# Kernel tuning notes

Hardware: AMD Instinct MI355X
Metric: run time of the kernel (lower is better)

The kernel has to match this reference:

```python
import jax, jax.numpy as jnp
import numpy as np

SCALE = 64.0
MARGIN = 0.5
COS_M = float(np.cos(MARGIN))
SIN_M = float(np.sin(MARGIN))
TH = float(np.cos(np.pi - MARGIN))
MM = float(np.sin(np.pi - MARGIN) * MARGIN)
B, D, C = 1024, 512, 50000


def setup_inputs() -> dict:
    key = jax.random.key(0)
    k1, k2, k3 = jax.random.split(key, 3)
    embeddings = jax.random.normal(k1, (B, D), dtype=jnp.float32)
    labels = jax.random.randint(k2, (B,), 0, C, dtype=jnp.int32)
    # xavier_uniform over (num_classes, embedding_dim)
    limit = float(np.sqrt(6.0 / (C + D)))
    weight = jax.random.uniform(k3, (C, D), dtype=jnp.float32, minval=-limit, maxval=limit)
    return {"embeddings": embeddings, "labels": labels, "weight": weight}


def _l2norm(x, axis=-1, eps=1e-12):
    # matches F.normalize(p=2): x / max(||x||, eps)
    n = jnp.sqrt(jnp.sum(x * x, axis=axis, keepdims=True))
    return x / jnp.maximum(n, eps)


def reference(embeddings, labels, weight):
    e = _l2norm(embeddings, axis=1)          # [B, D]
    w = _l2norm(weight, axis=1)              # [C, D]
    cosine = jnp.einsum('bd,cd->bc', e, w)   # [B, C]
    sine = jnp.sqrt(1.0 - jnp.clip(cosine * cosine, 0.0, 1.0))
    phi = cosine * COS_M - sine * SIN_M
    phi = jnp.where(cosine > TH, phi, cosine - MM)
    one_hot = jax.nn.one_hot(labels, cosine.shape[1], dtype=cosine.dtype)
    logits = SCALE * (one_hot * phi + (1.0 - one_hot) * cosine)
    # cross_entropy with integer labels, mean reduction
    logp = jax.nn.log_softmax(logits, axis=1)
    nll = -jnp.take_along_axis(logp, labels[:, None].astype(jnp.int32), axis=1)[:, 0]
    return jnp.mean(nll)
```

## Files before the change

### kernel.cpp

```cpp
#include <hip/hip_runtime.h>
#include <hip/hip_bf16.h>
#include <cstdint>

#define BB 1024
#define DD 512
#define CC 50000
#define CCP 50048
#define NTN 782
#define NBLK 512
#define SCALE_F 64.0f
#define LOG2E_F 1.44269504088896340736f
#define SCALE_L2E_F (SCALE_F * LOG2E_F)
#define COS_M_F 0.87758256189037276f
#define SIN_M_F 0.47942553860420301f
#define TH_F   (-0.87758256189037276f)
#define MM_F   0.23971276930210156f

typedef __attribute__((ext_vector_type(4))) int i32x4;
typedef __attribute__((ext_vector_type(8))) char char8;

#define OFF_RS   ((size_t)0)
#define OFF_ES   (OFF_RS + 4096)
#define OFF_WS   (OFF_ES + 4096)
#define OFF_EI8  (OFF_WS + 204800)
#define OFF_WI8  (OFF_EI8 + (size_t)BB*DD)

__global__ void quant_kernel(const float* __restrict__ emb, const float* __restrict__ wgt,
                             char* __restrict__ ei8, float* __restrict__ es,
                             char* __restrict__ wi8, float* __restrict__ wsc,
                             float* __restrict__ rowsum, float* __restrict__ out) {
    const int blk = blockIdx.x;
    if (blk == 12756) {
        const int t = threadIdx.x;
        #pragma unroll
        for (int i = 0; i < 4; ++i) rowsum[i * 256 + t] = 0.f;
        if (t == 0) out[0] = 0.f;
        int4* pz = reinterpret_cast<int4*>(wi8 + (size_t)CC * DD + t * 96);
        #pragma unroll
        for (int i = 0; i < 6; ++i) pz[i] = (int4){0, 0, 0, 0};
        if (t < CCP - CC) wsc[CC + t] = 0.f;
        return;
    }
    const int r4 = threadIdx.x >> 6;
    const int l  = threadIdx.x & 63;
    const bool isw = blk < 12500;
    const int row = isw ? (blk * 4 + r4) : ((blk - 12500) * 4 + r4);
    const float* src = (isw ? wgt : emb) + (size_t)row * DD;
    const float4* r = reinterpret_cast<const float4*>(src);
    float4 v0 = r[l * 2 + 0];
    float4 v1 = r[l * 2 + 1];
    float ss = v0.x*v0.x + v0.y*v0.y + v0.z*v0.z + v0.w*v0.w
             + v1.x*v1.x + v1.y*v1.y + v1.z*v1.z + v1.w*v1.w;
    float mx = fmaxf(fmaxf(fmaxf(fabsf(v0.x), fabsf(v0.y)), fmaxf(fabsf(v0.z), fabsf(v0.w))),
                     fmaxf(fmaxf(fabsf(v1.x), fabsf(v1.y)), fmaxf(fabsf(v1.z), fabsf(v1.w))));
    #pragma unroll
    for (int m = 1; m < 64; m <<= 1) {
        ss += __shfl_xor(ss, m);
        mx = fmaxf(mx, __shfl_xor(mx, m));
    }
    float nrm = fmaxf(sqrtf(ss), 1e-12f);
    float ma  = fmaxf(mx, 1e-20f);
    float qs  = 127.0f / ma;
    if (l == 0) (isw ? wsc : es)[row] = ma / (127.0f * nrm);
    char8 q;
    q[0]=(char)__float2int_rn(v0.x*qs); q[1]=(char)__float2int_rn(v0.y*qs);
    q[2]=(char)__float2int_rn(v0.z*qs); q[3]=(char)__float2int_rn(v0.w*qs);
    q[4]=(char)__float2int_rn(v1.x*qs); q[5]=(char)__float2int_rn(v1.y*qs);
    q[6]=(char)__float2int_rn(v1.z*qs); q[7]=(char)__float2int_rn(v1.w*qs);
    *reinterpret_cast<char8*>((isw ? wi8 : ei8) + (size_t)row * DD + l * 8) = q;
}

__global__ __launch_bounds__(512, 4) void arc_gemm_i8_kernel(
        const char* __restrict__ ei8,
        const char* __restrict__ wi8,
        const float* __restrict__ es,
        const float* __restrict__ wsc,
        float* __restrict__ rowsum)
{
    __shared__ __align__(16) char lds[2][32768];

    const int t   = threadIdx.x;
    const int wid = t >> 6;
    const int wm  = wid >> 1;
    const int wn  = wid & 1;
    const int l   = t & 63;
    const int r16 = l & 15;
    const int kg  = l >> 4;

    const int bid  = blockIdx.x;
    const int bidp = (bid & 7) * 64 + (bid >> 3);
    const int mt = bidp & 7;
    const int s  = bidp >> 3;
    const int m0 = mt * 128;
    const int nt0 = (s < 14) ? s * 13 : 12 * s + 14;
    const int cnt = (s < 14) ? 13 : 12;

    i32x4 af[2][8];
    #pragma unroll
    for (int fm = 0; fm < 2; ++fm)
        #pragma unroll
        for (int kk = 0; kk < 8; ++kk)
            af[fm][kk] = *reinterpret_cast<const i32x4*>(
                ei8 + (size_t)(m0 + wm * 32 + fm * 16 + r16) * DD + kk * 64 + kg * 16);

    float se_r[2][4];
    #pragma unroll
    for (int fm = 0; fm < 2; ++fm)
        #pragma unroll
        for (int j = 0; j < 4; ++j)
            se_r[fm][j] = es[m0 + wm * 32 + fm * 16 + kg * 4 + j];

    float rs[2][4];
    #pragma unroll
    for (int fm = 0; fm < 2; ++fm)
        #pragma unroll
        for (int j = 0; j < 4; ++j) rs[fm][j] = 0.f;

    const char* sp4[4];
    #pragma unroll
    for (int i = 0; i < 4; ++i) {
        int flat = (i * 512 + t) * 16;
        int kk2  = flat >> 13;
        int row  = (flat >> 7) & 63;
        int col  = flat & 127;
        int scol = col ^ ((row & 7) << 4);
        sp4[i] = wi8 + (size_t)(nt0 * 64 + row) * DD + kk2 * 128 + scol;
    }
    auto stageB = [&](int buf) {
        #pragma unroll
        for (int i = 0; i < 4; ++i) {
            __builtin_amdgcn_global_load_lds(
                (const __attribute__((address_space(1))) void*)sp4[i],
                (__attribute__((address_space(3))) void*)(&lds[buf][(i * 512 + t) * 16]),
                16, 0, 0);
            sp4[i] += 64 * DD;
        }
    };
    const float* wp = wsc + nt0 * 64 + wn * 32 + r16;

    stageB(0);
    asm volatile("s_waitcnt vmcnt(0)" ::: "memory");
    __builtin_amdgcn_s_barrier();

    for (int i = 0; i < cnt; ++i) {
        const int buf = i & 1;
        if (i + 1 < cnt) stageB(buf ^ 1);

        float sw_0 = wp[0]  * SCALE_L2E_F;
        float sw_1 = wp[16] * SCALE_L2E_F;
        wp += 64;

        i32x4 acc[2][2];
        #pragma unroll
        for (int fm = 0; fm < 2; ++fm)
            #pragma unroll
            for (int fn = 0; fn < 2; ++fn) acc[fm][fn] = (i32x4){0, 0, 0, 0};
        #pragma unroll
        for (int kk = 0; kk < 8; ++kk) {
            i32x4 b[2];
            #pragma unroll
            for (int fn = 0; fn < 2; ++fn) {
                int row = wn * 32 + fn * 16 + r16;
                int off = (kk >> 1) * 8192 + row * 128
                        + (((kk & 1) * 64 + kg * 16) ^ ((row & 7) << 4));
                b[fn] = *reinterpret_cast<const i32x4*>(&lds[buf][off]);
            }
            #pragma unroll
            for (int fm = 0; fm < 2; ++fm)
                #pragma unroll
                for (int fn = 0; fn < 2; ++fn)
                    acc[fm][fn] = __builtin_amdgcn_mfma_i32_16x16x64_i8(af[fm][kk], b[fn], acc[fm][fn], 0, 0, 0);
        }

        asm volatile("s_waitcnt vmcnt(0)" ::: "memory");
        __builtin_amdgcn_s_barrier();

        #pragma unroll
        for (int fm = 0; fm < 2; ++fm)
            #pragma unroll
            for (int j = 0; j < 4; ++j) {
                float k0 = se_r[fm][j] * sw_0;
                float k1 = se_r[fm][j] * sw_1;
                rs[fm][j] += exp2f(fmaf((float)acc[fm][0][j], k0, -SCALE_L2E_F));
                rs[fm][j] += exp2f(fmaf((float)acc[fm][1][j], k1, -SCALE_L2E_F));
            }
    }

    #pragma unroll
    for (int fm = 0; fm < 2; ++fm) {
        #pragma unroll
        for (int j = 0; j < 4; ++j) {
            float v = rs[fm][j];
            #pragma unroll
            for (int mk = 1; mk < 16; mk <<= 1) v += __shfl_xor(v, mk);
            if (r16 == 0) {
                int grow = m0 + wm * 32 + fm * 16 + kg * 4 + j;
                atomicAdd(&rowsum[grow], v);
            }
        }
    }
}

__global__ void finish_kernel(const char* __restrict__ ei8, const char* __restrict__ wi8,
                              const float* __restrict__ es, const float* __restrict__ wsc,
                              const int* __restrict__ labels,
                              const float* __restrict__ rowsum, float* __restrict__ out) {
    const int b = blockIdx.x;
    const int l = threadIdx.x;
    const int lab = labels[b];
    char8 a = *reinterpret_cast<const char8*>(ei8 + (size_t)b * DD + l * 8);
    char8 w = *reinterpret_cast<const char8*>(wi8 + (size_t)lab * DD + l * 8);
    int d = 0;
    #pragma unroll
    for (int k = 0; k < 8; ++k) d += (int)a[k] * (int)w[k];
    #pragma unroll
    for (int m = 1; m < 64; m <<= 1) d += __shfl_xor(d, m);
    if (l == 0) {
        float swl = wsc[lab] * SCALE_L2E_F;
        float kf  = es[b] * swl;
        float sub = exp2f(fmaf((float)d, kf, -SCALE_L2E_F));
        float cosv = (float)d * es[b] * wsc[lab];
        float c2 = fminf(fmaxf(cosv * cosv, 0.f), 1.f);
        float phi = cosv * COS_M_F - sqrtf(1.f - c2) * SIN_M_F;
        phi = (cosv > TH_F) ? phi : (cosv - MM_F);
        float ml = SCALE_F * phi;
        float Sf = rowsum[b] + __expf(ml - SCALE_F) - sub;
        float nll = -(ml - SCALE_F - logf(Sf));
        atomicAdd(out, nll * (1.0f / BB));
    }
}

extern "C" void kernel_launch(void* const* d_in, const int* in_sizes, int n_in,
                              void* d_out, int out_size, void* d_ws, size_t ws_size,
                              hipStream_t stream) {
    const float* emb    = (const float*)d_in[0];
    const int*   labels = (const int*)d_in[1];
    const float* wgt    = (const float*)d_in[2];
    float* out = (float*)d_out;
    char* ws = (char*)d_ws;

    float* rowsum = (float*)(ws + OFF_RS);
    float* es     = (float*)(ws + OFF_ES);
    float* wsc    = (float*)(ws + OFF_WS);
    char*  ei8    = (char*)(ws + OFF_EI8);
    char*  wi8    = (char*)(ws + OFF_WI8);

    quant_kernel<<<12757, 256, 0, stream>>>(emb, wgt, ei8, es, wi8, wsc, rowsum, out);
    arc_gemm_i8_kernel<<<NBLK, 512, 0, stream>>>(ei8, wi8, es, wsc, rowsum);
    finish_kernel<<<BB, 64, 0, stream>>>(ei8, wi8, es, wsc, labels, rowsum, out);
}
```

Before: 81.74 us.

## Drop LDS staging; load B fragments directly from global with smaller blocks

The GEMM kernel no longer stages weight tiles through double-buffered LDS with global_load_lds and barriers. Each wave now reads its B fragments straight from global memory into registers. Blocks shrink to 256 threads covering 32-column tiles, and the grid doubles to 1024 blocks. This removes LDS traffic and block-wide synchronisation, but there is no longer any prefetch overlap, and every wave in a block re-reads the same weight rows from global or L2 instead of sharing them.

```diff
diff --git a/kernel.cpp b/kernel.cpp
--- a/kernel.cpp
+++ b/kernel.cpp
@@ -6,8 +6,8 @@
 #define DD 512
 #define CC 50000
 #define CCP 50048
-#define NTN 782
-#define NBLK 512
+#define NCT 1564
+#define NBLK 1024
 #define SCALE_F 64.0f
 #define LOG2E_F 1.44269504088896340736f
 #define SCALE_L2E_F (SCALE_F * LOG2E_F)
@@ -70,30 +70,26 @@
     *reinterpret_cast<char8*>((isw ? wi8 : ei8) + (size_t)row * DD + l * 8) = q;
 }
 
-__global__ __launch_bounds__(512, 4) void arc_gemm_i8_kernel(
+__global__ __launch_bounds__(256, 4) void arc_gemm_i8_kernel(
         const char* __restrict__ ei8,
         const char* __restrict__ wi8,
         const float* __restrict__ es,
         const float* __restrict__ wsc,
         float* __restrict__ rowsum)
 {
-    __shared__ __align__(16) char lds[2][32768];
-
     const int t   = threadIdx.x;
     const int wid = t >> 6;
-    const int wm  = wid >> 1;
-    const int wn  = wid & 1;
     const int l   = t & 63;
     const int r16 = l & 15;
     const int kg  = l >> 4;
 
     const int bid  = blockIdx.x;
-    const int bidp = (bid & 7) * 64 + (bid >> 3);
+    const int bidp = (bid & 7) * 128 + (bid >> 3);
     const int mt = bidp & 7;
     const int s  = bidp >> 3;
-    const int m0 = mt * 128;
-    const int nt0 = (s < 14) ? s * 13 : 12 * s + 14;
-    const int cnt = (s < 14) ? 13 : 12;
+    const int rowb = mt * 128 + wid * 32;
+    const int nt0 = (s < 28) ? s * 13 : 12 * s + 28;
+    const int cnt = (s < 28) ? 13 : 12;
 
     i32x4 af[2][8];
     #pragma unroll
@@ -101,14 +97,14 @@
         #pragma unroll
         for (int kk = 0; kk < 8; ++kk)
             af[fm][kk] = *reinterpret_cast<const i32x4*>(
-                ei8 + (size_t)(m0 + wm * 32 + fm * 16 + r16) * DD + kk * 64 + kg * 16);
+                ei8 + (size_t)(rowb + fm * 16 + r16) * DD + kk * 64 + kg * 16);
 
     float se_r[2][4];
     #pragma unroll
     for (int fm = 0; fm < 2; ++fm)
         #pragma unroll
         for (int j = 0; j < 4; ++j)
-            se_r[fm][j] = es[m0 + wm * 32 + fm * 16 + kg * 4 + j];
+            se_r[fm][j] = es[rowb + fm * 16 + kg * 4 + j];
 
     float rs[2][4];
     #pragma unroll
@@ -116,64 +112,32 @@
         #pragma unroll
         for (int j = 0; j < 4; ++j) rs[fm][j] = 0.f;
 
-    const char* sp4[4];
-    #pragma unroll
-    for (int i = 0; i < 4; ++i) {
-        int flat = (i * 512 + t) * 16;
-        int kk2  = flat >> 13;
-        int row  = (flat >> 7) & 63;
-        int col  = flat & 127;
-        int scol = col ^ ((row & 7) << 4);
-        sp4[i] = wi8 + (size_t)(nt0 * 64 + row) * DD + kk2 * 128 + scol;
-    }
-    auto stageB = [&](int buf) {
-        #pragma unroll
-        for (int i = 0; i < 4; ++i) {
-            __builtin_amdgcn_global_load_lds(
-                (const __attribute__((address_space(1))) void*)sp4[i],
-                (__attribute__((address_space(3))) void*)(&lds[buf][(i * 512 + t) * 16]),
-                16, 0, 0);
-            sp4[i] += 64 * DD;
-        }
-    };
-    const float* wp = wsc + nt0 * 64 + wn * 32 + r16;
-
-    stageB(0);
-    asm volatile("s_waitcnt vmcnt(0)" ::: "memory");
-    __builtin_amdgcn_s_barrier();
+    const char* pb0 = wi8 + (size_t)(nt0 * 32 + r16) * DD + kg * 16;
+    const char* pb1 = pb0 + 16 * DD;
+    const float* wp = wsc + nt0 * 32 + r16;
 
     for (int i = 0; i < cnt; ++i) {
-        const int buf = i & 1;
-        if (i + 1 < cnt) stageB(buf ^ 1);
-
         float sw_0 = wp[0]  * SCALE_L2E_F;
         float sw_1 = wp[16] * SCALE_L2E_F;
-        wp += 64;
+        wp += 32;
 
         i32x4 acc[2][2];
         #pragma unroll
         for (int fm = 0; fm < 2; ++fm)
             #pragma unroll
             for (int fn = 0; fn < 2; ++fn) acc[fm][fn] = (i32x4){0, 0, 0, 0};
+
         #pragma unroll
         for (int kk = 0; kk < 8; ++kk) {
-            i32x4 b[2];
-            #pragma unroll
-            for (int fn = 0; fn < 2; ++fn) {
-                int row = wn * 32 + fn * 16 + r16;
-                int off = (kk >> 1) * 8192 + row * 128
-                        + (((kk & 1) * 64 + kg * 16) ^ ((row & 7) << 4));
-                b[fn] = *reinterpret_cast<const i32x4*>(&lds[buf][off]);
-            }
-            #pragma unroll
-            for (int fm = 0; fm < 2; ++fm)
-                #pragma unroll
-                for (int fn = 0; fn < 2; ++fn)
-                    acc[fm][fn] = __builtin_amdgcn_mfma_i32_16x16x64_i8(af[fm][kk], b[fn], acc[fm][fn], 0, 0, 0);
+            i32x4 b0 = *reinterpret_cast<const i32x4*>(pb0 + kk * 64);
+            i32x4 b1 = *reinterpret_cast<const i32x4*>(pb1 + kk * 64);
+            acc[0][0] = __builtin_amdgcn_mfma_i32_16x16x64_i8(af[0][kk], b0, acc[0][0], 0, 0, 0);
+            acc[1][0] = __builtin_amdgcn_mfma_i32_16x16x64_i8(af[1][kk], b0, acc[1][0], 0, 0, 0);
+            acc[0][1] = __builtin_amdgcn_mfma_i32_16x16x64_i8(af[0][kk], b1, acc[0][1], 0, 0, 0);
+            acc[1][1] = __builtin_amdgcn_mfma_i32_16x16x64_i8(af[1][kk], b1, acc[1][1], 0, 0, 0);
         }
-
-        asm volatile("s_waitcnt vmcnt(0)" ::: "memory");
-        __builtin_amdgcn_s_barrier();
+        pb0 += 32 * DD;
+        pb1 += 32 * DD;
 
         #pragma unroll
         for (int fm = 0; fm < 2; ++fm)
@@ -194,7 +158,7 @@
             #pragma unroll
             for (int mk = 1; mk < 16; mk <<= 1) v += __shfl_xor(v, mk);
             if (r16 == 0) {
-                int grow = m0 + wm * 32 + fm * 16 + kg * 4 + j;
+                int grow = rowb + fm * 16 + kg * 4 + j;
                 atomicAdd(&rowsum[grow], v);
             }
         }
@@ -246,6 +210,6 @@
     char*  wi8    = (char*)(ws + OFF_WI8);
 
     quant_kernel<<<12757, 256, 0, stream>>>(emb, wgt, ei8, es, wi8, wsc, rowsum, out);
-    arc_gemm_i8_kernel<<<NBLK, 512, 0, stream>>>(ei8, wi8, es, wsc, rowsum);
+    arc_gemm_i8_kernel<<<NBLK, 256, 0, stream>>>(ei8, wi8, es, wsc, rowsum);
     finish_kernel<<<BB, 64, 0, stream>>>(ei8, wi8, es, wsc, labels, rowsum, out);
 }
```

Measured after the change: 142.8 us. 74.7% more time.
